# Kernel optimization log

Hardware: AMD Instinct MI355X
Metric: run time of the kernel (lower is better)

## Reference

```python
import jax, jax.numpy as jnp
import numpy as np

N_NODES = 100_000
N_EDGES = 3_200_000
N_GRAPHS = 256
F_IN = 128


def setup_inputs() -> dict:
    key = jax.random.key(0)
    ks = jax.random.split(key, 12)
    x = jax.random.normal(ks[0], (N_NODES, F_IN), dtype=jnp.float32)
    edge_weight = jax.random.uniform(ks[1], (N_EDGES,), dtype=jnp.float32)
    W1 = jax.random.normal(ks[2], (F_IN, 16), dtype=jnp.float32) * (1.0 / np.sqrt(F_IN))
    b1 = jnp.zeros((16,), jnp.float32)
    W2 = jax.random.normal(ks[3], (16, 16), dtype=jnp.float32) * 0.25
    b2 = jnp.zeros((16,), jnp.float32)
    Wd2 = jax.random.normal(ks[4], (16, 16), dtype=jnp.float32) * 0.25
    bd2 = jnp.zeros((16,), jnp.float32)
    Wd3 = jax.random.normal(ks[5], (16, 2), dtype=jnp.float32) * 0.25
    bd3 = jnp.zeros((2,), jnp.float32)
    row = jax.random.randint(ks[6], (N_EDGES,), 0, N_NODES, dtype=jnp.int32)
    col = jax.random.randint(ks[7], (N_EDGES,), 0, N_NODES, dtype=jnp.int32)
    seg = jnp.sort(jax.random.randint(ks[8], (N_NODES,), 0, N_GRAPHS, dtype=jnp.int32))
    return {"x": x, "edge_weight": edge_weight, "W1": W1, "b1": b1, "W2": W2,
            "b2": b2, "Wd2": Wd2, "bd2": bd2, "Wd3": Wd3, "bd3": bd3,
            "row": row, "col": col, "seg": seg}


def _gcn_conv(x, row, col, w, kernel, bias):
    # Spektral GCNConv: out = A_norm @ (x @ kernel) + bias
    h = x @ kernel                                   # [N, C]
    msg = h[col] * w[:, None]                        # gather + weight, [E, C]
    agg = jax.ops.segment_sum(msg, row, num_segments=N_NODES)  # scatter-add
    return agg + bias


def reference(x, edge_weight, W1, b1, W2, b2, Wd2, bd2, Wd3, bd3, row, col, seg):
    h = jax.nn.elu(_gcn_conv(x, row, col, edge_weight, W1, b1))
    h = jax.nn.elu(_gcn_conv(h, row, col, edge_weight, W2, b2))
    pooled = jax.ops.segment_sum(h, seg, num_segments=N_GRAPHS)  # [G, 16]
    out = jax.nn.relu(pooled @ Wd2 + bd2)
    # Dropout is identity at inference time
    out = jax.nn.sigmoid(out @ Wd3 + bd3)            # [G, 2]
    return out
```

## Files before the change

kernel.cpp:

```cpp
#include <hip/hip_runtime.h>

#define N_NODES 100000
#define N_EDGES 3200000
#define N_GRAPHS 256
#define F_IN 128
#define CH 16

__global__ __launch_bounds__(256) void gemm1_kernel(const float* __restrict__ x,
                                                    const float* __restrict__ W1,
                                                    float* __restrict__ out) {
    __shared__ float xs[16 * 128];
    __shared__ float w1s[128 * 16];
    const int tid = threadIdx.x;
    const int nb = blockIdx.x * 16;
#pragma unroll
    for (int i = 0; i < 8; ++i) w1s[tid + i * 256] = W1[tid + i * 256];
    const float* xsrc = x + (size_t)nb * 128;
#pragma unroll
    for (int i = 0; i < 8; ++i) xs[tid + i * 256] = xsrc[tid + i * 256];
    __syncthreads();
    const int ln = tid >> 4, oc = tid & 15;
    float acc = 0.f;
#pragma unroll 8
    for (int k = 0; k < 128; ++k)
        acc = fmaf(xs[ln * 128 + k], w1s[k * 16 + oc], acc);
    out[(size_t)(nb + ln) * 16 + oc] = acc;
}

__global__ __launch_bounds__(256) void gemm16_kernel(const float* __restrict__ h,
                                                     const float* __restrict__ W,
                                                     float* __restrict__ out) {
    __shared__ float hs[256];
    __shared__ float wsm[256];
    const int tid = threadIdx.x;
    const int nb = blockIdx.x * 16;
    wsm[tid] = W[tid];
    hs[tid] = h[(size_t)nb * 16 + tid];
    __syncthreads();
    const int ln = tid >> 4, oc = tid & 15;
    float acc = 0.f;
#pragma unroll
    for (int k = 0; k < 16; ++k)
        acc = fmaf(hs[ln * 16 + k], wsm[k * 16 + oc], acc);
    out[(size_t)(nb + ln) * 16 + oc] = acc;
}

__global__ __launch_bounds__(256) void scatter_kernel(const float* __restrict__ h,
                                                      const float* __restrict__ w,
                                                      const int* __restrict__ row,
                                                      const int* __restrict__ col,
                                                      float* __restrict__ agg) {
    const long long t = (long long)blockIdx.x * 256 + threadIdx.x;
    const int e = (int)(t >> 4);
    const int ch = (int)(t & 15);
    const int r = row[e], c = col[e];
    const float wt = w[e];
    const float v = h[(size_t)c * 16 + ch] * wt;
    atomicAdd(agg + (size_t)r * 16 + ch, v);
}

__global__ __launch_bounds__(256) void elubias_kernel(float* __restrict__ a,
                                                      const float* __restrict__ b) {
    __shared__ float bs[16];
    if (threadIdx.x < 16) bs[threadIdx.x] = b[threadIdx.x];
    __syncthreads();
    const int total = N_NODES * 16;
    for (int i = blockIdx.x * 256 + threadIdx.x; i < total; i += gridDim.x * 256) {
        float v = a[i] + bs[i & 15];
        a[i] = v > 0.f ? v : expm1f(v);
    }
}

#define POOL_NODES 1024
__global__ __launch_bounds__(256) void pool_kernel(const float* __restrict__ h,
                                                   const int* __restrict__ seg,
                                                   float* __restrict__ pooled) {
    __shared__ float lp[N_GRAPHS * 16];
    const int tid = threadIdx.x;
    for (int i = tid; i < N_GRAPHS * 16; i += 256) lp[i] = 0.f;
    __syncthreads();
    const int base = blockIdx.x * POOL_NODES;
    const int lim = min(base + POOL_NODES, N_NODES);
    for (int idx = base * 16 + tid; idx < lim * 16; idx += 256) {
        const int node = idx >> 4;
        const int ch = idx & 15;
        atomicAdd(&lp[seg[node] * 16 + ch], h[idx]);
    }
    __syncthreads();
    const int s0 = seg[base];
    const int s1 = seg[lim - 1];
    const int cnt = (s1 - s0 + 1) * 16;
    for (int j = tid; j < cnt; j += 256) {
        atomicAdd(&pooled[s0 * 16 + j], lp[s0 * 16 + j]);
    }
}

__global__ __launch_bounds__(256) void head_kernel(const float* __restrict__ pooled,
                                                   const float* __restrict__ Wd2,
                                                   const float* __restrict__ bd2,
                                                   const float* __restrict__ Wd3,
                                                   const float* __restrict__ bd3,
                                                   float* __restrict__ out) {
    __shared__ float w2[256], w3[32], b2s[16], b3s[2];
    const int tid = threadIdx.x;
    w2[tid] = Wd2[tid];
    if (tid < 32) w3[tid] = Wd3[tid];
    if (tid < 16) b2s[tid] = bd2[tid];
    if (tid < 2) b3s[tid] = bd3[tid];
    __syncthreads();
    const int g = tid;
    float p[16];
#pragma unroll
    for (int k = 0; k < 16; ++k) p[k] = pooled[g * 16 + k];
    float t[16];
#pragma unroll
    for (int j = 0; j < 16; ++j) {
        float acc = b2s[j];
#pragma unroll
        for (int k = 0; k < 16; ++k) acc = fmaf(p[k], w2[k * 16 + j], acc);
        t[j] = acc > 0.f ? acc : 0.f;
    }
#pragma unroll
    for (int m = 0; m < 2; ++m) {
        float acc = b3s[m];
#pragma unroll
        for (int j = 0; j < 16; ++j) acc = fmaf(t[j], w3[j * 2 + m], acc);
        out[g * 2 + m] = 1.f / (1.f + expf(-acc));
    }
}

extern "C" void kernel_launch(void* const* d_in, const int* in_sizes, int n_in,
                              void* d_out, int out_size, void* d_ws, size_t ws_size,
                              hipStream_t stream) {
    const float* x   = (const float*)d_in[0];
    const float* ew  = (const float*)d_in[1];
    const float* W1  = (const float*)d_in[2];
    const float* b1  = (const float*)d_in[3];
    const float* W2  = (const float*)d_in[4];
    const float* b2  = (const float*)d_in[5];
    const float* Wd2 = (const float*)d_in[6];
    const float* bd2 = (const float*)d_in[7];
    const float* Wd3 = (const float*)d_in[8];
    const float* bd3 = (const float*)d_in[9];
    const int* row   = (const int*)d_in[10];
    const int* col   = (const int*)d_in[11];
    const int* seg   = (const int*)d_in[12];
    float* out = (float*)d_out;

    float* A = (float*)d_ws;
    float* B = A + (size_t)N_NODES * 16;
    float* pooled = B + (size_t)N_NODES * 16;

    const size_t h_bytes = (size_t)N_NODES * 16 * sizeof(float);
    const int scatter_blocks = (int)(((long long)N_EDGES * 16) / 256);

    gemm1_kernel<<<N_NODES / 16, 256, 0, stream>>>(x, W1, A);
    hipMemsetAsync(B, 0, h_bytes, stream);
    scatter_kernel<<<scatter_blocks, 256, 0, stream>>>(A, ew, row, col, B);
    elubias_kernel<<<2048, 256, 0, stream>>>(B, b1);

    gemm16_kernel<<<N_NODES / 16, 256, 0, stream>>>(B, W2, A);
    hipMemsetAsync(B, 0, h_bytes, stream);
    scatter_kernel<<<scatter_blocks, 256, 0, stream>>>(A, ew, row, col, B);
    elubias_kernel<<<2048, 256, 0, stream>>>(B, b2);

    hipMemsetAsync(pooled, 0, N_GRAPHS * 16 * sizeof(float), stream);
    pool_kernel<<<(N_NODES + POOL_NODES - 1) / POOL_NODES, 256, 0, stream>>>(B, seg, pooled);
    head_kernel<<<1, 256, 0, stream>>>(pooled, Wd2, bd2, Wd3, bd3, out);
}
```

Before: 529.4 us.

## Build CSR by row per call and replace atomic scatter with pull aggregation

Each call builds a CSR adjacency: it histograms row indices, runs a three-stage prefix scan, and atomically fills packed (col, weight) entries. The two scatter-add passes become pull kernels, one wavefront per node, with bias and ELU folded in. This removes 51.2M float atomics per layer and the memsets and separate elementwise passes. In exchange it adds a 3.2M-int atomic histogram and fill pass, several small launches, and extra workspace, with a fallback to the old path if the workspace is too small.

Result: slower. 688.7 us (+30.1%).

```diff
diff --git a/kernel.cpp b/kernel.cpp
--- a/kernel.cpp
+++ b/kernel.cpp
@@ -3,8 +3,6 @@
 #define N_NODES 100000
 #define N_EDGES 3200000
 #define N_GRAPHS 256
-#define F_IN 128
-#define CH 16
 
 __global__ __launch_bounds__(256) void gemm1_kernel(const float* __restrict__ x,
                                                     const float* __restrict__ W1,
@@ -43,6 +41,119 @@
     for (int k = 0; k < 16; ++k)
         acc = fmaf(hs[ln * 16 + k], wsm[k * 16 + oc], acc);
     out[(size_t)(nb + ln) * 16 + oc] = acc;
+}
+
+__global__ __launch_bounds__(256) void hist_kernel(const int* __restrict__ row,
+                                                   int* __restrict__ cnt) {
+    const int e = blockIdx.x * 256 + threadIdx.x;
+    atomicAdd(&cnt[row[e]], 1);
+}
+
+#define SCAN_CHUNK 1024
+#define NB1 98
+
+__global__ __launch_bounds__(256) void scanA_kernel(const int* __restrict__ cnt,
+                                                    int* __restrict__ bsum) {
+    __shared__ int part[256];
+    const int b = blockIdx.x, t = threadIdx.x;
+    const int base = b * SCAN_CHUNK + t * 4;
+    int s = 0;
+#pragma unroll
+    for (int i = 0; i < 4; ++i) { int idx = base + i; s += (idx < N_NODES) ? cnt[idx] : 0; }
+    part[t] = s; __syncthreads();
+    for (int off = 128; off > 0; off >>= 1) {
+        if (t < off) part[t] += part[t + off];
+        __syncthreads();
+    }
+    if (t == 0) bsum[b] = part[0];
+}
+
+__global__ __launch_bounds__(128) void scanB_kernel(const int* __restrict__ bsum,
+                                                    int* __restrict__ boff,
+                                                    int* __restrict__ ptr) {
+    __shared__ int a[128];
+    const int t = threadIdx.x;
+    const int v = (t < NB1) ? bsum[t] : 0;
+    a[t] = v; __syncthreads();
+    for (int off = 1; off < 128; off <<= 1) {
+        int u = (t >= off) ? a[t - off] : 0;
+        __syncthreads();
+        a[t] += u;
+        __syncthreads();
+    }
+    if (t < NB1) boff[t] = a[t] - v;
+    if (t == 0) ptr[N_NODES] = N_EDGES;
+}
+
+__global__ __launch_bounds__(256) void scanC_kernel(const int* __restrict__ cnt,
+                                                    const int* __restrict__ boff,
+                                                    int* __restrict__ ptr,
+                                                    int* __restrict__ cur) {
+    __shared__ int a[256];
+    const int b = blockIdx.x, t = threadIdx.x;
+    const int base = b * SCAN_CHUNK + t * 4;
+    const int c0 = (base + 0 < N_NODES) ? cnt[base + 0] : 0;
+    const int c1 = (base + 1 < N_NODES) ? cnt[base + 1] : 0;
+    const int c2 = (base + 2 < N_NODES) ? cnt[base + 2] : 0;
+    const int c3 = (base + 3 < N_NODES) ? cnt[base + 3] : 0;
+    const int s = c0 + c1 + c2 + c3;
+    a[t] = s; __syncthreads();
+    for (int off = 1; off < 256; off <<= 1) {
+        int u = (t >= off) ? a[t - off] : 0;
+        __syncthreads();
+        a[t] += u;
+        __syncthreads();
+    }
+    int ex = a[t] - s + boff[b];
+    const int p0 = ex, p1 = ex + c0, p2 = p1 + c1, p3 = p2 + c2;
+    if (base + 0 < N_NODES) { ptr[base + 0] = p0; cur[base + 0] = p0; }
+    if (base + 1 < N_NODES) { ptr[base + 1] = p1; cur[base + 1] = p1; }
+    if (base + 2 < N_NODES) { ptr[base + 2] = p2; cur[base + 2] = p2; }
+    if (base + 3 < N_NODES) { ptr[base + 3] = p3; cur[base + 3] = p3; }
+}
+
+__global__ __launch_bounds__(256) void fill_kernel(const int* __restrict__ row,
+                                                   const int* __restrict__ col,
+                                                   const float* __restrict__ ew,
+                                                   int* __restrict__ cur,
+                                                   float2* __restrict__ ent) {
+    const int e = blockIdx.x * 256 + threadIdx.x;
+    const int r = row[e];
+    const int pos = atomicAdd(&cur[r], 1);
+    float2 v;
+    v.x = __int_as_float(col[e]);
+    v.y = ew[e];
+    ent[pos] = v;
+}
+
+__global__ __launch_bounds__(256) void pull_kernel(const float* __restrict__ h,
+                                                   const float2* __restrict__ ent,
+                                                   const int* __restrict__ ptr,
+                                                   const float* __restrict__ bias,
+                                                   float* __restrict__ out) {
+    const int wid = (blockIdx.x * 256 + threadIdx.x) >> 6;
+    if (wid >= N_NODES) return;
+    const int lane = threadIdx.x & 63;
+    const int ch = lane & 15, slot = lane >> 4;
+    const int beg = ptr[wid], end = ptr[wid + 1];
+    float acc = 0.f;
+    int e = beg + slot;
+    for (; e + 4 < end; e += 8) {
+        const float2 a0 = ent[e];
+        const float2 a1 = ent[e + 4];
+        acc += h[(size_t)__float_as_int(a0.x) * 16 + ch] * a0.y;
+        acc += h[(size_t)__float_as_int(a1.x) * 16 + ch] * a1.y;
+    }
+    if (e < end) {
+        const float2 a0 = ent[e];
+        acc += h[(size_t)__float_as_int(a0.x) * 16 + ch] * a0.y;
+    }
+    acc += __shfl_xor(acc, 16);
+    acc += __shfl_xor(acc, 32);
+    if (lane < 16) {
+        const float v = acc + bias[ch];
+        out[(size_t)wid * 16 + lane] = v > 0.f ? v : expm1f(v);
+    }
 }
 
 __global__ __launch_bounds__(256) void scatter_kernel(const float* __restrict__ h,
@@ -147,24 +258,57 @@
     const int* seg   = (const int*)d_in[12];
     float* out = (float*)d_out;
 
-    float* A = (float*)d_ws;
-    float* B = A + (size_t)N_NODES * 16;
-    float* pooled = B + (size_t)N_NODES * 16;
-
-    const size_t h_bytes = (size_t)N_NODES * 16 * sizeof(float);
-    const int scatter_blocks = (int)(((long long)N_EDGES * 16) / 256);
-
-    gemm1_kernel<<<N_NODES / 16, 256, 0, stream>>>(x, W1, A);
-    hipMemsetAsync(B, 0, h_bytes, stream);
-    scatter_kernel<<<scatter_blocks, 256, 0, stream>>>(A, ew, row, col, B);
-    elubias_kernel<<<2048, 256, 0, stream>>>(B, b1);
-
-    gemm16_kernel<<<N_NODES / 16, 256, 0, stream>>>(B, W2, A);
-    hipMemsetAsync(B, 0, h_bytes, stream);
-    scatter_kernel<<<scatter_blocks, 256, 0, stream>>>(A, ew, row, col, B);
-    elubias_kernel<<<2048, 256, 0, stream>>>(B, b2);
-
-    hipMemsetAsync(pooled, 0, N_GRAPHS * 16 * sizeof(float), stream);
-    pool_kernel<<<(N_NODES + POOL_NODES - 1) / POOL_NODES, 256, 0, stream>>>(B, seg, pooled);
-    head_kernel<<<1, 256, 0, stream>>>(pooled, Wd2, bd2, Wd3, bd3, out);
-}
+    char* wsc = (char*)d_ws;
+    const size_t ENT_B = (size_t)N_EDGES * 8;
+    float2* ent   = (float2*)wsc;
+    float*  A     = (float*)(wsc + ENT_B);
+    float*  B     = (float*)(wsc + ENT_B + 6400000);
+    float*  pooled= (float*)(wsc + ENT_B + 12800000);
+    int*    ptr   = (int*)  (wsc + ENT_B + 12816384);
+    int*    cnt   = (int*)  (wsc + ENT_B + 13216388);
+    int*    cur   = (int*)  (wsc + ENT_B + 13616388);
+    int*    bsum  = (int*)  (wsc + ENT_B + 14016388);
+    int*    boff  = (int*)  (wsc + ENT_B + 14016780);
+    const size_t REQ = ENT_B + 14017172;
+
+    const int EB = N_EDGES / 256;
+
+    if (ws_size >= REQ) {
+        hipMemsetAsync(cnt, 0, (size_t)N_NODES * 4, stream);
+        hist_kernel<<<EB, 256, 0, stream>>>(row, cnt);
+        scanA_kernel<<<NB1, 256, 0, stream>>>(cnt, bsum);
+        scanB_kernel<<<1, 128, 0, stream>>>(bsum, boff, ptr);
+        scanC_kernel<<<NB1, 256, 0, stream>>>(cnt, boff, ptr, cur);
+        fill_kernel<<<EB, 256, 0, stream>>>(row, col, ew, cur, ent);
+
+        gemm1_kernel<<<N_NODES / 16, 256, 0, stream>>>(x, W1, A);
+        pull_kernel<<<(N_NODES * 64) / 256, 256, 0, stream>>>(A, ent, ptr, b1, B);
+
+        gemm16_kernel<<<N_NODES / 16, 256, 0, stream>>>(B, W2, A);
+        pull_kernel<<<(N_NODES * 64) / 256, 256, 0, stream>>>(A, ent, ptr, b2, B);
+
+        hipMemsetAsync(pooled, 0, N_GRAPHS * 16 * sizeof(float), stream);
+        pool_kernel<<<(N_NODES + POOL_NODES - 1) / POOL_NODES, 256, 0, stream>>>(B, seg, pooled);
+        head_kernel<<<1, 256, 0, stream>>>(pooled, Wd2, bd2, Wd3, bd3, out);
+    } else {
+        float* fA = (float*)d_ws;
+        float* fB = fA + (size_t)N_NODES * 16;
+        float* fpooled = fB + (size_t)N_NODES * 16;
+        const size_t h_bytes = (size_t)N_NODES * 16 * sizeof(float);
+        const int scatter_blocks = (int)(((long long)N_EDGES * 16) / 256);
+
+        gemm1_kernel<<<N_NODES / 16, 256, 0, stream>>>(x, W1, fA);
+        hipMemsetAsync(fB, 0, h_bytes, stream);
+        scatter_kernel<<<scatter_blocks, 256, 0, stream>>>(fA, ew, row, col, fB);
+        elubias_kernel<<<2048, 256, 0, stream>>>(fB, b1);
+
+        gemm16_kernel<<<N_NODES / 16, 256, 0, stream>>>(fB, W2, fA);
+        hipMemsetAsync(fB, 0, h_bytes, stream);
+        scatter_kernel<<<scatter_blocks, 256, 0, stream>>>(fA, ew, row, col, fB);
+        elubias_kernel<<<2048, 256, 0, stream>>>(fB, b2);
+
+        hipMemsetAsync(fpooled, 0, N_GRAPHS * 16 * sizeof(float), stream);
+        pool_kernel<<<(N_NODES + POOL_NODES - 1) / POOL_NODES, 256, 0, stream>>>(fB, seg, fpooled);
+        head_kernel<<<1, 256, 0, stream>>>(fpooled, Wd2, bd2, Wd3, bd3, out);
+    }
+}
```

## Bucket edges by destination row and aggregate in shared memory

Applied to the files above, without the earlier changes.

Each call now runs a counting-sort pass (histogram, two scans, partition) that groups the edges into 391 buckets of 256 destination nodes. Each edge is packed with its local row, source column and weight. A new aggregation kernel gives one 1024-thread block per bucket, accumulates messages with shared-memory atomics, and applies bias plus ELU on write-out. This removes the global atomics, the memsets and the separate elementwise passes. In exchange it adds a partition pass over all edges each call and runs only one block per bucket, which may limit occupancy. The old path is kept as a fallback when the workspace is too small.

Result: slower. 914.4 us (+72.7%).

```diff
diff --git a/kernel.cpp b/kernel.cpp
--- a/kernel.cpp
+++ b/kernel.cpp
@@ -3,8 +3,10 @@
 #define N_NODES 100000
 #define N_EDGES 3200000
 #define N_GRAPHS 256
-#define F_IN 128
-#define CH 16
+
+#define NBKT 391
+#define EBLK 782
+#define ECHUNK 4096
 
 __global__ __launch_bounds__(256) void gemm1_kernel(const float* __restrict__ x,
                                                     const float* __restrict__ W1,
@@ -43,6 +45,148 @@
     for (int k = 0; k < 16; ++k)
         acc = fmaf(hs[ln * 16 + k], wsm[k * 16 + oc], acc);
     out[(size_t)(nb + ln) * 16 + oc] = acc;
+}
+
+__global__ __launch_bounds__(256) void ghist_kernel(const int* __restrict__ row,
+                                                    int* __restrict__ blockhist) {
+    __shared__ int lh[NBKT];
+    const int tid = threadIdx.x, blk = blockIdx.x;
+    for (int i = tid; i < NBKT; i += 256) lh[i] = 0;
+    __syncthreads();
+    const int ebase = blk * ECHUNK;
+#pragma unroll
+    for (int j = 0; j < 16; ++j) {
+        const int e = ebase + j * 256 + tid;
+        if (e < N_EDGES) atomicAdd(&lh[row[e] >> 8], 1);
+    }
+    __syncthreads();
+    for (int i = tid; i < NBKT; i += 256) blockhist[i * EBLK + blk] = lh[i];
+}
+
+__global__ __launch_bounds__(1024) void scanbkt_kernel(const int* __restrict__ blockhist,
+                                                       int* __restrict__ cursors,
+                                                       int* __restrict__ total) {
+    __shared__ int a[1024];
+    const int t = threadIdx.x, b = blockIdx.x;
+    const int c = (t < EBLK) ? blockhist[b * EBLK + t] : 0;
+    a[t] = c; __syncthreads();
+    for (int off = 1; off < 1024; off <<= 1) {
+        const int v = (t >= off) ? a[t - off] : 0;
+        __syncthreads(); a[t] += v; __syncthreads();
+    }
+    if (t < EBLK) cursors[b * EBLK + t] = a[t] - c;
+    if (t == 1023) total[b] = a[1023];
+}
+
+__global__ __launch_bounds__(512) void scanbase_kernel(const int* __restrict__ total,
+                                                       int* __restrict__ base) {
+    __shared__ int a[512];
+    const int t = threadIdx.x;
+    const int v = (t < NBKT) ? total[t] : 0;
+    a[t] = v; __syncthreads();
+    for (int off = 1; off < 512; off <<= 1) {
+        const int u = (t >= off) ? a[t - off] : 0;
+        __syncthreads(); a[t] += u; __syncthreads();
+    }
+    if (t < NBKT) base[t] = a[t] - v;
+    if (t == 511) base[NBKT] = a[511];
+}
+
+__global__ __launch_bounds__(256) void partition_kernel(const int* __restrict__ row,
+                                                        const int* __restrict__ col,
+                                                        const float* __restrict__ ew,
+                                                        const int* __restrict__ cursors,
+                                                        const int* __restrict__ gbase,
+                                                        uint2* __restrict__ ent) {
+    __shared__ int lhist[NBKT];
+    __shared__ int wbase[NBKT];
+    __shared__ int stmp[256];
+    __shared__ uint2 sent[ECHUNK];
+    __shared__ unsigned short sbkt[ECHUNK];
+    const int tid = threadIdx.x, blk = blockIdx.x;
+    for (int i = tid; i < NBKT; i += 256) lhist[i] = 0;
+    __syncthreads();
+    const int ebase = blk * ECHUNK;
+    unsigned meta[16], exv[16];
+    float wv[16];
+#pragma unroll
+    for (int j = 0; j < 16; ++j) {
+        const int e = ebase + j * 256 + tid;
+        meta[j] = 0xFFFFFFFFu;
+        if (e < N_EDGES) {
+            const int r = row[e];
+            const int bkt = r >> 8;
+            const int lr = atomicAdd(&lhist[bkt], 1);
+            meta[j] = ((unsigned)bkt << 12) | (unsigned)lr;
+            exv[j] = ((unsigned)(r & 255) << 17) | (unsigned)col[e];
+            wv[j] = ew[e];
+        }
+    }
+    __syncthreads();
+    const int i0 = 2 * tid, i1 = 2 * tid + 1;
+    const int s0 = (i0 < NBKT) ? lhist[i0] : 0;
+    const int s1 = (i1 < NBKT) ? lhist[i1] : 0;
+    const int s = s0 + s1;
+    stmp[tid] = s; __syncthreads();
+    for (int off = 1; off < 256; off <<= 1) {
+        const int u = (tid >= off) ? stmp[tid - off] : 0;
+        __syncthreads(); stmp[tid] += u; __syncthreads();
+    }
+    const int pre = stmp[tid] - s;
+    if (i0 < NBKT) {
+        wbase[i0] = gbase[i0] + cursors[i0 * EBLK + blk] - pre;
+        lhist[i0] = pre;
+    }
+    if (i1 < NBKT) {
+        wbase[i1] = gbase[i1] + cursors[i1 * EBLK + blk] - (pre + s0);
+        lhist[i1] = pre + s0;
+    }
+    __syncthreads();
+#pragma unroll
+    for (int j = 0; j < 16; ++j) {
+        if (meta[j] != 0xFFFFFFFFu) {
+            const int bkt = meta[j] >> 12;
+            const int lr = meta[j] & 4095;
+            const int slot = lhist[bkt] + lr;
+            sent[slot] = make_uint2(exv[j], __float_as_uint(wv[j]));
+            sbkt[slot] = (unsigned short)bkt;
+        }
+    }
+    __syncthreads();
+    const int ve = min(ECHUNK, N_EDGES - ebase);
+    for (int s2 = tid; s2 < ve; s2 += 256) {
+        const int b = sbkt[s2];
+        ent[wbase[b] + s2] = sent[s2];
+    }
+}
+
+__global__ __launch_bounds__(1024) void agg_kernel(const float* __restrict__ h,
+                                                   const uint2* __restrict__ ent,
+                                                   const int* __restrict__ gbase,
+                                                   const float* __restrict__ bias,
+                                                   float* __restrict__ out) {
+    __shared__ float agg[256 * 16];
+    const int tid = threadIdx.x, bkt = blockIdx.x;
+    for (int i = tid; i < 4096; i += 1024) agg[i] = 0.f;
+    __syncthreads();
+    const int start = gbase[bkt], end = gbase[bkt + 1];
+    const int ch = tid & 15;
+    for (int i = start + (tid >> 4); i < end; i += 64) {
+        const uint2 e = ent[i];
+        const int rl = (e.x >> 17) & 255;
+        const int c  = e.x & 0x1FFFF;
+        const float w = __uint_as_float(e.y);
+        atomicAdd(&agg[(rl << 4) | ch], h[(size_t)c * 16 + ch] * w);
+    }
+    __syncthreads();
+    const int node0 = bkt << 8;
+    for (int k = tid; k < 4096; k += 1024) {
+        const int node = node0 + (k >> 4);
+        if (node < N_NODES) {
+            const float v = agg[k] + bias[k & 15];
+            out[(size_t)node * 16 + (k & 15)] = v > 0.f ? v : expm1f(v);
+        }
+    }
 }
 
 __global__ __launch_bounds__(256) void scatter_kernel(const float* __restrict__ h,
@@ -55,8 +199,7 @@
     const int ch = (int)(t & 15);
     const int r = row[e], c = col[e];
     const float wt = w[e];
-    const float v = h[(size_t)c * 16 + ch] * wt;
-    atomicAdd(agg + (size_t)r * 16 + ch, v);
+    atomicAdd(agg + (size_t)r * 16 + ch, h[(size_t)c * 16 + ch] * wt);
 }
 
 __global__ __launch_bounds__(256) void elubias_kernel(float* __restrict__ a,
@@ -82,9 +225,7 @@
     const int base = blockIdx.x * POOL_NODES;
     const int lim = min(base + POOL_NODES, N_NODES);
     for (int idx = base * 16 + tid; idx < lim * 16; idx += 256) {
-        const int node = idx >> 4;
-        const int ch = idx & 15;
-        atomicAdd(&lp[seg[node] * 16 + ch], h[idx]);
+        atomicAdd(&lp[seg[idx >> 4] * 16 + (idx & 15)], h[idx]);
     }
     __syncthreads();
     const int s0 = seg[base];
@@ -147,24 +288,52 @@
     const int* seg   = (const int*)d_in[12];
     float* out = (float*)d_out;
 
-    float* A = (float*)d_ws;
-    float* B = A + (size_t)N_NODES * 16;
-    float* pooled = B + (size_t)N_NODES * 16;
-
-    const size_t h_bytes = (size_t)N_NODES * 16 * sizeof(float);
-    const int scatter_blocks = (int)(((long long)N_EDGES * 16) / 256);
-
-    gemm1_kernel<<<N_NODES / 16, 256, 0, stream>>>(x, W1, A);
-    hipMemsetAsync(B, 0, h_bytes, stream);
-    scatter_kernel<<<scatter_blocks, 256, 0, stream>>>(A, ew, row, col, B);
-    elubias_kernel<<<2048, 256, 0, stream>>>(B, b1);
-
-    gemm16_kernel<<<N_NODES / 16, 256, 0, stream>>>(B, W2, A);
-    hipMemsetAsync(B, 0, h_bytes, stream);
-    scatter_kernel<<<scatter_blocks, 256, 0, stream>>>(A, ew, row, col, B);
-    elubias_kernel<<<2048, 256, 0, stream>>>(B, b2);
-
-    hipMemsetAsync(pooled, 0, N_GRAPHS * 16 * sizeof(float), stream);
-    pool_kernel<<<(N_NODES + POOL_NODES - 1) / POOL_NODES, 256, 0, stream>>>(B, seg, pooled);
-    head_kernel<<<1, 256, 0, stream>>>(pooled, Wd2, bd2, Wd3, bd3, out);
-}
+    char* wsc = (char*)d_ws;
+    const size_t ENT_B = (size_t)N_EDGES * 8;
+    uint2* ent      = (uint2*)wsc;
+    int*   blockhist= (int*)(wsc + ENT_B);
+    int*   cursors  = (int*)(wsc + ENT_B + 1223048);
+    float* A        = (float*)(wsc + ENT_B);
+    float* B        = (float*)(wsc + ENT_B + 6400000);
+    float* pooled   = (float*)(wsc + ENT_B + 12800000);
+    int*   total    = (int*)(wsc + ENT_B + 12816384);
+    int*   gbase    = (int*)(wsc + ENT_B + 12817948);
+    const size_t REQ = ENT_B + 12819516;
+
+    if (ws_size >= REQ) {
+        ghist_kernel<<<EBLK, 256, 0, stream>>>(row, blockhist);
+        scanbkt_kernel<<<NBKT, 1024, 0, stream>>>(blockhist, cursors, total);
+        scanbase_kernel<<<1, 512, 0, stream>>>(total, gbase);
+        partition_kernel<<<EBLK, 256, 0, stream>>>(row, col, ew, cursors, gbase, ent);
+
+        gemm1_kernel<<<N_NODES / 16, 256, 0, stream>>>(x, W1, A);
+        agg_kernel<<<NBKT, 1024, 0, stream>>>(A, ent, gbase, b1, B);
+
+        gemm16_kernel<<<N_NODES / 16, 256, 0, stream>>>(B, W2, A);
+        agg_kernel<<<NBKT, 1024, 0, stream>>>(A, ent, gbase, b2, B);
+
+        hipMemsetAsync(pooled, 0, N_GRAPHS * 16 * sizeof(float), stream);
+        pool_kernel<<<(N_NODES + POOL_NODES - 1) / POOL_NODES, 256, 0, stream>>>(B, seg, pooled);
+        head_kernel<<<1, 256, 0, stream>>>(pooled, Wd2, bd2, Wd3, bd3, out);
+    } else {
+        float* fA = (float*)d_ws;
+        float* fB = fA + (size_t)N_NODES * 16;
+        float* fpooled = fB + (size_t)N_NODES * 16;
+        const size_t h_bytes = (size_t)N_NODES * 16 * sizeof(float);
+        const int scatter_blocks = (int)(((long long)N_EDGES * 16) / 256);
+
+        gemm1_kernel<<<N_NODES / 16, 256, 0, stream>>>(x, W1, fA);
+        hipMemsetAsync(fB, 0, h_bytes, stream);
+        scatter_kernel<<<scatter_blocks, 256, 0, stream>>>(fA, ew, row, col, fB);
+        elubias_kernel<<<2048, 256, 0, stream>>>(fB, b1);
+
+        gemm16_kernel<<<N_NODES / 16, 256, 0, stream>>>(fB, W2, fA);
+        hipMemsetAsync(fB, 0, h_bytes, stream);
+        scatter_kernel<<<scatter_blocks, 256, 0, stream>>>(fA, ew, row, col, fB);
+        elubias_kernel<<<2048, 256, 0, stream>>>(fB, b2);
+
+        hipMemsetAsync(fpooled, 0, N_GRAPHS * 16 * sizeof(float), stream);
+        pool_kernel<<<(N_NODES + POOL_NODES - 1) / POOL_NODES, 256, 0, stream>>>(fB, seg, fpooled);
+        head_kernel<<<1, 256, 0, stream>>>(fpooled, Wd2, bd2, Wd3, bd3, out);
+    }
+}
```
